# Kernel optimization log

Hardware: AMD Instinct MI355X
Metric: run time of the kernel (lower is better)

## Reference

```python
import jax, jax.numpy as jnp
import numpy as np

N_NODES = 100000
N_EDGES = 1600000
IN, HID, OUT = 32, 32, 16


def setup_inputs() -> dict:
    key = jax.random.key(0)
    ks = jax.random.split(key, 8)
    return {
        "features": jax.random.normal(ks[0], (N_NODES, IN), dtype=jnp.float32),
        "src": jax.random.randint(ks[1], (N_EDGES,), 0, N_NODES, dtype=jnp.int32),
        "dst": jax.random.randint(ks[2], (N_EDGES,), 0, N_NODES, dtype=jnp.int32),
        "edge_weight": jax.random.uniform(ks[3], (N_EDGES,), dtype=jnp.float32),
        "W1": jax.random.normal(ks[4], (IN, HID), dtype=jnp.float32) * 0.1,
        "b1": jnp.zeros((HID,), dtype=jnp.float32),
        "W2": jax.random.normal(ks[5], (HID, OUT), dtype=jnp.float32) * 0.1,
        "b2": jnp.zeros((OUT,), dtype=jnp.float32),
    }


def _graph_conv(h, W, b, src, dst, edge_weight, norm_src, norm_dst, n):
    # DGL GraphConv, norm='both', with edge_weight (u_mul_e aggregation)
    h = h * norm_src[:, None]          # out-degree^-0.5 on source side
    h = h @ W                          # dense transform (tiny GEMM)
    m = h[src] * edge_weight[:, None]  # gather + edge weighting  [E, d]
    agg = jax.ops.segment_sum(m, dst, num_segments=n)  # scatter-add SpMM
    return agg * norm_dst[:, None] + b # in-degree^-0.5 + bias


def reference(features, src, dst, edge_weight, W1, b1, W2, b2):
    n = features.shape[0]
    ones_e = jnp.ones_like(edge_weight)
    deg_out = jnp.clip(jax.ops.segment_sum(ones_e, src, num_segments=n), 1.0)
    deg_in = jnp.clip(jax.ops.segment_sum(ones_e, dst, num_segments=n), 1.0)
    norm_src = deg_out ** -0.5
    norm_dst = deg_in ** -0.5
    h = _graph_conv(features, W1, b1, src, dst, edge_weight, norm_src, norm_dst, n)
    h = jax.nn.relu(h)
    # dropout is identity in eval mode
    h = _graph_conv(h, W2, b2, src, dst, edge_weight, norm_src, norm_dst, n)
    return h
```

## Files before the change

### kernel.cpp

```cpp
#include <hip/hip_runtime.h>
#include <hip/hip_fp16.h>


#define NB   391
#define CAPB 5504
#define EPB  4096

__device__ __forceinline__ long nt_load_i64(const long* p) {
    return __builtin_nontemporal_load(p);
}

__global__ __launch_bounds__(512) void partition_kernel(
        const int* __restrict__ src, const int* __restrict__ dst,
        const float* __restrict__ ew,
        int* __restrict__ g_cur_d, int* __restrict__ g_cur_s,
        int2* __restrict__ pack_part, unsigned char* __restrict__ src_part, int m) {
    __shared__ int hist_d[NB], hist_s[NB];
    __shared__ int lbase_d[NB], lbase_s[NB];
    __shared__ int gbase_d[NB], gbase_s[NB];
    __shared__ int cur_d[NB], cur_s[NB];
    __shared__ int sc[2][512];
    __shared__ long stage[EPB];
    __shared__ unsigned short dbuck[EPB];
    __shared__ unsigned char  sstage[EPB];
    __shared__ unsigned short sbuck[EPB];
    int t = threadIdx.x;
    for (int i = t; i < NB; i += 512) {
        hist_d[i] = 0; hist_s[i] = 0; cur_d[i] = 0; cur_s[i] = 0;
    }
    __syncthreads();
    int base_e = blockIdx.x * EPB;
    int total = m - base_e; if (total > EPB) total = EPB;
    int es[8], ed[8]; float wv[8];
#pragma unroll
    for (int k = 0; k < 8; k++) {
        int e = base_e + k * 512 + t;
        if (e < m) { es[k] = src[e]; ed[k] = dst[e]; wv[k] = ew[e]; }
        else ed[k] = -1;
    }
#pragma unroll
    for (int k = 0; k < 8; k++) {
        if (ed[k] >= 0) {
            atomicAdd(&hist_d[ed[k] >> 8], 1);
            atomicAdd(&hist_s[es[k] >> 8], 1);
        }
    }
    __syncthreads();
    if (t < 512) sc[0][t] = (t < NB) ? hist_d[t] : 0;
    __syncthreads();
    int pp = 0;
    for (int off = 1; off < 512; off <<= 1) {
        sc[1 - pp][t] = sc[pp][t] + (t >= off ? sc[pp][t - off] : 0);
        __syncthreads();
        pp ^= 1;
    }
    for (int i = t; i < NB; i += 512) lbase_d[i] = sc[pp][i] - hist_d[i];
    __syncthreads();
    sc[0][t] = (t < NB) ? hist_s[t] : 0;
    __syncthreads();
    pp = 0;
    for (int off = 1; off < 512; off <<= 1) {
        sc[1 - pp][t] = sc[pp][t] + (t >= off ? sc[pp][t - off] : 0);
        __syncthreads();
        pp ^= 1;
    }
    for (int i = t; i < NB; i += 512) lbase_s[i] = sc[pp][i] - hist_s[i];
    __syncthreads();
    for (int i = t; i < NB; i += 512) {
        int c = hist_d[i];
        gbase_d[i] = i * CAPB + (c ? atomicAdd(&g_cur_d[i], c) : 0);
        c = hist_s[i];
        gbase_s[i] = i * CAPB + (c ? atomicAdd(&g_cur_s[i], c) : 0);
    }
    __syncthreads();
#pragma unroll
    for (int k = 0; k < 8; k++) {
        if (ed[k] >= 0) {
            int d = ed[k], s = es[k];
            int bd = d >> 8;
            int r = atomicAdd(&cur_d[bd], 1);
            int pos = lbase_d[bd] + r;
            stage[pos] = (long)(unsigned int)(s | ((d & 255) << 20)) |
                         ((long)__float_as_int(wv[k]) << 32);
            dbuck[pos] = (unsigned short)bd;
            int bs = s >> 8;
            int rs = atomicAdd(&cur_s[bs], 1);
            int ps = lbase_s[bs] + rs;
            sstage[ps] = (unsigned char)(s & 255);
            sbuck[ps] = (unsigned short)bs;
        }
    }
    __syncthreads();
    long* packl = (long*)pack_part;
    for (int i = t; i < total; i += 512) {
        int b = dbuck[i];
        packl[(size_t)gbase_d[b] + (i - lbase_d[b])] = stage[i];
    }
    for (int i = t; i < total; i += 512) {
        int b = sbuck[i];
        src_part[(size_t)gbase_s[b] + (i - lbase_s[b])] = sstage[i];
    }
}

__global__ __launch_bounds__(1024) void csr_kernel(
                           const int2* __restrict__ pack_part,
                           const unsigned char* __restrict__ src_part,
                           const int* __restrict__ g_cur_d, const int* __restrict__ g_cur_s,
                           const float* __restrict__ feat, const float* __restrict__ W1,
                           int2* __restrict__ csr, int2* __restrict__ rs_cnt,
                           float* __restrict__ norm_src, float* __restrict__ norm_dst,
                           __half* __restrict__ h1, int n) {
    __shared__ int cnt[256];
    __shared__ int rowx[256];
    __shared__ int cur[256];
    __shared__ int cnt_s[256];
    __shared__ float nsrc[256];
    __shared__ float sW1[1024];
    extern __shared__ int2 stage[];
    int t = threadIdx.x, b = blockIdx.x;
    if (t < 256) { cnt[t] = 0; cur[t] = 0; cnt_s[t] = 0; }
    sW1[t] = W1[t];
    __syncthreads();
    int count = g_cur_d[b]; if (count > CAPB) count = CAPB;
    int count_s = g_cur_s[b]; if (count_s > CAPB) count_s = CAPB;
    const int2* p = pack_part + (size_t)b * CAPB;
    const unsigned char* sp = src_part + (size_t)b * CAPB;
    for (int e = t; e < count; e += 1024) atomicAdd(&cnt[p[e].x >> 20], 1);
    for (int e = t; e < count_s; e += 1024) atomicAdd(&cnt_s[sp[e]], 1);
    __syncthreads();
    if (t < 256) {
        int node = b * 256 + t;
        if (node < n) {
            int cs = cnt_s[t];
            float ns = rsqrtf((float)(cs > 1 ? cs : 1));
            nsrc[t] = ns;
            norm_src[node] = ns;
        } else nsrc[t] = 0.0f;
    }
    int c0 = 0;
    if (t < 256) { c0 = cnt[t]; rowx[t] = c0; }
    __syncthreads();
    for (int off = 1; off < 256; off <<= 1) {
        int v = 0;
        if (t < 256 && t >= off) v = rowx[t - off];
        __syncthreads();
        if (t < 256) rowx[t] += v;
        __syncthreads();
    }
    if (t < 256) {
        int excl = rowx[t] - c0;
        rowx[t] = excl;
        int node = b * 256 + t;
        if (node < n) {
            rs_cnt[node] = make_int2(b * CAPB + excl, c0);
            norm_dst[node] = rsqrtf((float)(c0 > 1 ? c0 : 1));
        }
    }
    __syncthreads();
    for (int e = t; e < count; e += 1024) {
        int2 v = p[e];
        int dl = v.x >> 20;
        int r = atomicAdd(&cur[dl], 1);
        stage[rowx[dl] + r] = make_int2(v.x & 0x1FFFF, v.y);
    }
    __syncthreads();
    int2* outp = csr + (size_t)b * CAPB;
    for (int e = t; e < count; e += 1024) outp[e] = stage[e];
    __syncthreads();
    float* sF = (float*)stage;
    int node0 = b * 256;
    int lim = n - node0; if (lim > 256) lim = 256; if (lim < 0) lim = 0;
    for (int o = t; o < lim * 32; o += 1024) {
        int i = o >> 5, k = o & 31;
        sF[o] = feat[(size_t)(node0 + i) * 32 + k] * nsrc[i];
    }
    __syncthreads();
    for (int o = t; o < lim * 32; o += 1024) {
        int i = o >> 5, col = o & 31;
        float acc = 0.0f;
#pragma unroll
        for (int k = 0; k < 32; k++) acc += sF[i * 32 + k] * sW1[k * 32 + col];
        h1[(size_t)(node0 + i) * 32 + col] = __float2half(acc);
    }
}

__global__ void gather1_fused_kernel(const __half* __restrict__ h1, const int2* __restrict__ csr,
                                     const int2* __restrict__ rs_cnt,
                                     const float* __restrict__ norm_src, const float* __restrict__ norm_dst,
                                     const float* __restrict__ W2, const float* __restrict__ b1,
                                     __half* __restrict__ h2, int n) {
    __shared__ float sW2[32 * 16];
    __shared__ float sB1[32];
    __shared__ float sX[4][8][32];
    int t = threadIdx.x;
    for (int i = t; i < 512; i += 256) sW2[i] = W2[i];
    if (t < 32) sB1[t] = b1[t];
    __syncthreads();
    int w = t >> 6, lane = t & 63;
    int q = lane >> 3;
    int dq = lane & 7;
    int node = (blockIdx.x * 4 + w) * 8 + q;
    bool valid = node < n;
    int2 rc = valid ? rs_cnt[node] : make_int2(0, 0);
    long base = rc.x;
    int c = rc.y;
    const float2* tv = (const float2*)h1;
    const long* csrl = (const long*)csr;
    float a00=0,a01=0,a02=0,a03=0, a10=0,a11=0,a12=0,a13=0;
    float a20=0,a21=0,a22=0,a23=0, a30=0,a31=0,a32=0,a33=0;
    int j = 0;
    for (; j + 3 < c; j += 4) {
        long q0 = nt_load_i64(csrl + base + j);
        long q1 = nt_load_i64(csrl + base + j + 1);
        long q2 = nt_load_i64(csrl + base + j + 2);
        long q3 = nt_load_i64(csrl + base + j + 3);
        float2 r0 = tv[(size_t)((int)q0 & 0xFFFFF) * 8 + dq];
        float2 r1 = tv[(size_t)((int)q1 & 0xFFFFF) * 8 + dq];
        float2 r2 = tv[(size_t)((int)q2 & 0xFFFFF) * 8 + dq];
        float2 r3 = tv[(size_t)((int)q3 & 0xFFFFF) * 8 + dq];
        float w0 = __int_as_float((int)(q0 >> 32)), w1 = __int_as_float((int)(q1 >> 32));
        float w2 = __int_as_float((int)(q2 >> 32)), w3 = __int_as_float((int)(q3 >> 32));
        float2 l0 = __half22float2(*(__half2*)&r0.x), h0 = __half22float2(*(__half2*)&r0.y);
        float2 l1 = __half22float2(*(__half2*)&r1.x), h1v = __half22float2(*(__half2*)&r1.y);
        float2 l2 = __half22float2(*(__half2*)&r2.x), h2v = __half22float2(*(__half2*)&r2.y);
        float2 l3 = __half22float2(*(__half2*)&r3.x), h3v = __half22float2(*(__half2*)&r3.y);
        a00 += l0.x * w0; a01 += l0.y * w0; a02 += h0.x * w0; a03 += h0.y * w0;
        a10 += l1.x * w1; a11 += l1.y * w1; a12 += h1v.x * w1; a13 += h1v.y * w1;
        a20 += l2.x * w2; a21 += l2.y * w2; a22 += h2v.x * w2; a23 += h2v.y * w2;
        a30 += l3.x * w3; a31 += l3.y * w3; a32 += h3v.x * w3; a33 += h3v.y * w3;
    }
    for (; j < c; j++) {
        long qq = nt_load_i64(csrl + base + j);
        float2 r = tv[(size_t)((int)qq & 0xFFFFF) * 8 + dq];
        float ww = __int_as_float((int)(qq >> 32));
        float2 l = __half22float2(*(__half2*)&r.x), h = __half22float2(*(__half2*)&r.y);
        a00 += l.x * ww; a01 += l.y * ww; a02 += h.x * ww; a03 += h.y * ww;
    }
    float s0 = (a00 + a10) + (a20 + a30);
    float s1 = (a01 + a11) + (a21 + a31);
    float s2 = (a02 + a12) + (a22 + a32);
    float s3 = (a03 + a13) + (a23 + a33);
    if (valid) {
        float nd = norm_dst[node], ns = norm_src[node];
        int d0 = 4 * dq;
        sX[w][q][d0]     = fmaxf(s0 * nd + sB1[d0],     0.0f) * ns;
        sX[w][q][d0 + 1] = fmaxf(s1 * nd + sB1[d0 + 1], 0.0f) * ns;
        sX[w][q][d0 + 2] = fmaxf(s2 * nd + sB1[d0 + 2], 0.0f) * ns;
        sX[w][q][d0 + 3] = fmaxf(s3 * nd + sB1[d0 + 3], 0.0f) * ns;
    }
    if (valid) {
        float o0 = 0.0f, o1 = 0.0f;
        int c0 = 2 * dq, c1 = 2 * dq + 1;
#pragma unroll
        for (int k = 0; k < 32; k++) {
            float x = sX[w][q][k];
            o0 += x * sW2[k * 16 + c0];
            o1 += x * sW2[k * 16 + c1];
        }
        ((__half2*)h2)[(size_t)node * 8 + dq] = __floats2half2_rn(o0, o1);
    }
}

__global__ void gather2_kernel(const __half* __restrict__ h2, const int2* __restrict__ csr,
                               const int2* __restrict__ rs_cnt,
                               const float* __restrict__ norm_dst, const float* __restrict__ b2,
                               float* __restrict__ out, int n) {
    int t = threadIdx.x;
    int w = t >> 6, lane = t & 63;
    int q = lane >> 2;
    int dq = lane & 3;
    int node = (blockIdx.x * 4 + w) * 16 + q;
    bool valid = node < n;
    int2 rc = valid ? rs_cnt[node] : make_int2(0, 0);
    long base = rc.x;
    int c = rc.y;
    const float2* tv = (const float2*)h2;
    const long* csrl = (const long*)csr;
    float a00=0,a01=0,a02=0,a03=0, a10=0,a11=0,a12=0,a13=0;
    float a20=0,a21=0,a22=0,a23=0, a30=0,a31=0,a32=0,a33=0;
    int j = 0;
    for (; j + 3 < c; j += 4) {
        long q0 = nt_load_i64(csrl + base + j);
        long q1 = nt_load_i64(csrl + base + j + 1);
        long q2 = nt_load_i64(csrl + base + j + 2);
        long q3 = nt_load_i64(csrl + base + j + 3);
        float2 r0 = tv[(size_t)((int)q0 & 0xFFFFF) * 4 + dq];
        float2 r1 = tv[(size_t)((int)q1 & 0xFFFFF) * 4 + dq];
        float2 r2 = tv[(size_t)((int)q2 & 0xFFFFF) * 4 + dq];
        float2 r3 = tv[(size_t)((int)q3 & 0xFFFFF) * 4 + dq];
        float w0 = __int_as_float((int)(q0 >> 32)), w1 = __int_as_float((int)(q1 >> 32));
        float w2 = __int_as_float((int)(q2 >> 32)), w3 = __int_as_float((int)(q3 >> 32));
        float2 l0 = __half22float2(*(__half2*)&r0.x), h0 = __half22float2(*(__half2*)&r0.y);
        float2 l1 = __half22float2(*(__half2*)&r1.x), h1v = __half22float2(*(__half2*)&r1.y);
        float2 l2 = __half22float2(*(__half2*)&r2.x), h2v = __half22float2(*(__half2*)&r2.y);
        float2 l3 = __half22float2(*(__half2*)&r3.x), h3v = __half22float2(*(__half2*)&r3.y);
        a00 += l0.x * w0; a01 += l0.y * w0; a02 += h0.x * w0; a03 += h0.y * w0;
        a10 += l1.x * w1; a11 += l1.y * w1; a12 += h1v.x * w1; a13 += h1v.y * w1;
        a20 += l2.x * w2; a21 += l2.y * w2; a22 += h2v.x * w2; a23 += h2v.y * w2;
        a30 += l3.x * w3; a31 += l3.y * w3; a32 += h3v.x * w3; a33 += h3v.y * w3;
    }
    for (; j < c; j++) {
        long qq = nt_load_i64(csrl + base + j);
        float2 r = tv[(size_t)((int)qq & 0xFFFFF) * 4 + dq];
        float ww = __int_as_float((int)(qq >> 32));
        float2 l = __half22float2(*(__half2*)&r.x), h = __half22float2(*(__half2*)&r.y);
        a00 += l.x * ww; a01 += l.y * ww; a02 += h.x * ww; a03 += h.y * ww;
    }
    if (valid) {
        float nd = norm_dst[node];
        int d0 = 4 * dq;
        float4 o;
        o.x = ((a00 + a10) + (a20 + a30)) * nd + b2[d0];
        o.y = ((a01 + a11) + (a21 + a31)) * nd + b2[d0 + 1];
        o.z = ((a02 + a12) + (a22 + a32)) * nd + b2[d0 + 2];
        o.w = ((a03 + a13) + (a23 + a33)) * nd + b2[d0 + 3];
        ((float4*)out)[(size_t)node * 4 + dq] = o;
    }
}

extern "C" void kernel_launch(void* const* d_in, const int* in_sizes, int n_in,
                              void* d_out, int out_size, void* d_ws, size_t ws_size,
                              hipStream_t stream) {
    const float* feat = (const float*)d_in[0];
    const int*   src  = (const int*)d_in[1];
    const int*   dst  = (const int*)d_in[2];
    const float* ew   = (const float*)d_in[3];
    const float* W1   = (const float*)d_in[4];
    const float* b1   = (const float*)d_in[5];
    const float* W2   = (const float*)d_in[6];
    const float* b2   = (const float*)d_in[7];
    float* out = (float*)d_out;

    const int n = in_sizes[0] / 32;
    const int m = in_sizes[1];

    char* wsb = (char*)d_ws;
    int2*   pack_part = (int2*)wsb;
    int2*   csr       = pack_part + (size_t)NB * CAPB;
    __half* h1        = (__half*)(csr + (size_t)NB * CAPB);
    __half* h2        = h1 + 32 * (size_t)n;
    float*  norm_src  = (float*)(h2 + 16 * (size_t)n);
    float*  norm_dst  = norm_src + n;
    int2*   rs_cnt    = (int2*)(norm_dst + n);
    int*    g_cur_d   = (int*)(rs_cnt + n);
    int*    g_cur_s   = g_cur_d + NB;
    unsigned char* src_part = (unsigned char*)(g_cur_s + NB);

    hipMemsetAsync(g_cur_d, 0, 2 * NB * sizeof(int), stream);

    partition_kernel<<<(m + EPB - 1) / EPB, 512, 0, stream>>>(src, dst, ew, g_cur_d, g_cur_s,
                                                              pack_part, src_part, m);
    csr_kernel<<<NB, 1024, CAPB * sizeof(int2), stream>>>(pack_part, src_part, g_cur_d, g_cur_s,
                                                          feat, W1, csr, rs_cnt,
                                                          norm_src, norm_dst, h1, n);
    gather1_fused_kernel<<<(n + 31) / 32, 256, 0, stream>>>(h1, csr, rs_cnt,
                                                            norm_src, norm_dst, W2, b1, h2, n);
    gather2_kernel<<<(n + 63) / 64, 256, 0, stream>>>(h2, csr, rs_cnt, norm_dst, b2, out, n);
}
```

Measured before the change: 186.7 us.

## Sort nodes by in-degree within each block to balance gather warp work

The CSR build now counting-sorts the 256 destination nodes of each partition by in-degree (capped at 63) and writes a permutation array plus row info in that sorted order. Both gather kernels walk the permuted slots, so the node groups sharing a wavefront have similar edge counts and less lane divergence from unequal loop trip counts. In exchange there is an extra indirection load, scattered output writes through the permutation, a serial 64-bin scan in thread 0, and launches sized to the padded slot count.

```diff
diff --git a/kernel.cpp b/kernel.cpp
--- a/kernel.cpp
+++ b/kernel.cpp
@@ -5,6 +5,7 @@
 #define NB   391
 #define CAPB 5504
 #define EPB  4096
+#define NSLOT (NB * 256)
 
 __device__ __forceinline__ long nt_load_i64(const long* p) {
     return __builtin_nontemporal_load(p);
@@ -108,6 +109,7 @@
                            const int* __restrict__ g_cur_d, const int* __restrict__ g_cur_s,
                            const float* __restrict__ feat, const float* __restrict__ W1,
                            int2* __restrict__ csr, int2* __restrict__ rs_cnt,
+                           int* __restrict__ perm,
                            float* __restrict__ norm_src, float* __restrict__ norm_dst,
                            __half* __restrict__ h1, int n) {
     __shared__ int cnt[256];
@@ -116,9 +118,11 @@
     __shared__ int cnt_s[256];
     __shared__ float nsrc[256];
     __shared__ float sW1[1024];
+    __shared__ int dbin[64], dcur[64], dbase[64];
     extern __shared__ int2 stage[];
     int t = threadIdx.x, b = blockIdx.x;
     if (t < 256) { cnt[t] = 0; cur[t] = 0; cnt_s[t] = 0; }
+    if (t >= 256 && t < 320) { dbin[t - 256] = 0; dcur[t - 256] = 0; }
     sW1[t] = W1[t];
     __syncthreads();
     int count = g_cur_d[b]; if (count > CAPB) count = CAPB;
@@ -147,14 +151,27 @@
         if (t < 256) rowx[t] += v;
         __syncthreads();
     }
+    int excl = 0, bin = 0;
     if (t < 256) {
-        int excl = rowx[t] - c0;
+        excl = rowx[t] - c0;
         rowx[t] = excl;
+        bin = c0 < 63 ? c0 : 63;
+        atomicAdd(&dbin[bin], 1);
         int node = b * 256 + t;
-        if (node < n) {
-            rs_cnt[node] = make_int2(b * CAPB + excl, c0);
-            norm_dst[node] = rsqrtf((float)(c0 > 1 ? c0 : 1));
-        }
+        if (node < n) norm_dst[node] = rsqrtf((float)(c0 > 1 ? c0 : 1));
+    }
+    __syncthreads();
+    if (t == 0) {
+        int s = 0;
+        for (int i = 0; i < 64; i++) { dbase[i] = s; s += dbin[i]; }
+    }
+    __syncthreads();
+    if (t < 256) {
+        int rank = dbase[bin] + atomicAdd(&dcur[bin], 1);
+        int gpos = b * 256 + rank;
+        int node = b * 256 + t;
+        rs_cnt[gpos] = make_int2(b * CAPB + excl, c0);
+        perm[gpos] = (node < n) ? node : -1;
     }
     __syncthreads();
     for (int e = t; e < count; e += 1024) {
@@ -185,10 +202,10 @@
 }
 
 __global__ void gather1_fused_kernel(const __half* __restrict__ h1, const int2* __restrict__ csr,
-                                     const int2* __restrict__ rs_cnt,
+                                     const int2* __restrict__ rs_cnt, const int* __restrict__ perm,
                                      const float* __restrict__ norm_src, const float* __restrict__ norm_dst,
                                      const float* __restrict__ W2, const float* __restrict__ b1,
-                                     __half* __restrict__ h2, int n) {
+                                     __half* __restrict__ h2) {
     __shared__ float sW2[32 * 16];
     __shared__ float sB1[32];
     __shared__ float sX[4][8][32];
@@ -199,9 +216,10 @@
     int w = t >> 6, lane = t & 63;
     int q = lane >> 3;
     int dq = lane & 7;
-    int node = (blockIdx.x * 4 + w) * 8 + q;
-    bool valid = node < n;
-    int2 rc = valid ? rs_cnt[node] : make_int2(0, 0);
+    int gid = (blockIdx.x * 4 + w) * 8 + q;
+    int pid = (gid < NSLOT) ? perm[gid] : -1;
+    bool valid = pid >= 0;
+    int2 rc = valid ? rs_cnt[gid] : make_int2(0, 0);
     long base = rc.x;
     int c = rc.y;
     const float2* tv = (const float2*)h1;
@@ -241,7 +259,7 @@
     float s2 = (a02 + a12) + (a22 + a32);
     float s3 = (a03 + a13) + (a23 + a33);
     if (valid) {
-        float nd = norm_dst[node], ns = norm_src[node];
+        float nd = norm_dst[pid], ns = norm_src[pid];
         int d0 = 4 * dq;
         sX[w][q][d0]     = fmaxf(s0 * nd + sB1[d0],     0.0f) * ns;
         sX[w][q][d0 + 1] = fmaxf(s1 * nd + sB1[d0 + 1], 0.0f) * ns;
@@ -257,21 +275,22 @@
             o0 += x * sW2[k * 16 + c0];
             o1 += x * sW2[k * 16 + c1];
         }
-        ((__half2*)h2)[(size_t)node * 8 + dq] = __floats2half2_rn(o0, o1);
+        ((__half2*)h2)[(size_t)pid * 8 + dq] = __floats2half2_rn(o0, o1);
     }
 }
 
 __global__ void gather2_kernel(const __half* __restrict__ h2, const int2* __restrict__ csr,
-                               const int2* __restrict__ rs_cnt,
+                               const int2* __restrict__ rs_cnt, const int* __restrict__ perm,
                                const float* __restrict__ norm_dst, const float* __restrict__ b2,
-                               float* __restrict__ out, int n) {
+                               float* __restrict__ out) {
     int t = threadIdx.x;
     int w = t >> 6, lane = t & 63;
     int q = lane >> 2;
     int dq = lane & 3;
-    int node = (blockIdx.x * 4 + w) * 16 + q;
-    bool valid = node < n;
-    int2 rc = valid ? rs_cnt[node] : make_int2(0, 0);
+    int gid = (blockIdx.x * 4 + w) * 16 + q;
+    int pid = (gid < NSLOT) ? perm[gid] : -1;
+    bool valid = pid >= 0;
+    int2 rc = valid ? rs_cnt[gid] : make_int2(0, 0);
     long base = rc.x;
     int c = rc.y;
     const float2* tv = (const float2*)h2;
@@ -307,14 +326,14 @@
         a00 += l.x * ww; a01 += l.y * ww; a02 += h.x * ww; a03 += h.y * ww;
     }
     if (valid) {
-        float nd = norm_dst[node];
+        float nd = norm_dst[pid];
         int d0 = 4 * dq;
         float4 o;
         o.x = ((a00 + a10) + (a20 + a30)) * nd + b2[d0];
         o.y = ((a01 + a11) + (a21 + a31)) * nd + b2[d0 + 1];
         o.z = ((a02 + a12) + (a22 + a32)) * nd + b2[d0 + 2];
         o.w = ((a03 + a13) + (a23 + a33)) * nd + b2[d0 + 3];
-        ((float4*)out)[(size_t)node * 4 + dq] = o;
+        ((float4*)out)[(size_t)pid * 4 + dq] = o;
     }
 }
 
@@ -342,7 +361,8 @@
     float*  norm_src  = (float*)(h2 + 16 * (size_t)n);
     float*  norm_dst  = norm_src + n;
     int2*   rs_cnt    = (int2*)(norm_dst + n);
-    int*    g_cur_d   = (int*)(rs_cnt + n);
+    int*    perm      = (int*)(rs_cnt + NSLOT);
+    int*    g_cur_d   = perm + NSLOT;
     int*    g_cur_s   = g_cur_d + NB;
     unsigned char* src_part = (unsigned char*)(g_cur_s + NB);
 
@@ -351,9 +371,10 @@
     partition_kernel<<<(m + EPB - 1) / EPB, 512, 0, stream>>>(src, dst, ew, g_cur_d, g_cur_s,
                                                               pack_part, src_part, m);
     csr_kernel<<<NB, 1024, CAPB * sizeof(int2), stream>>>(pack_part, src_part, g_cur_d, g_cur_s,
-                                                          feat, W1, csr, rs_cnt,
+                                                          feat, W1, csr, rs_cnt, perm,
                                                           norm_src, norm_dst, h1, n);
-    gather1_fused_kernel<<<(n + 31) / 32, 256, 0, stream>>>(h1, csr, rs_cnt,
-                                                            norm_src, norm_dst, W2, b1, h2, n);
-    gather2_kernel<<<(n + 63) / 64, 256, 0, stream>>>(h2, csr, rs_cnt, norm_dst, b2, out, n);
-}
+    gather1_fused_kernel<<<(NSLOT + 31) / 32, 256, 0, stream>>>(h1, csr, rs_cnt, perm,
+                                                                norm_src, norm_dst, W2, b1, h2);
+    gather2_kernel<<<(NSLOT + 63) / 64, 256, 0, stream>>>(h2, csr, rs_cnt, perm,
+                                                          norm_dst, b2, out);
+}
```

After: 205.0 us. 9.8% more time.
